# Kernel tuning notes

Hardware: AMD Instinct MI355X
Metric: run time of the kernel (lower is better)

Reference implementation:

```python
import jax, jax.numpy as jnp
import numpy as np

VIS_DIM, HID_DIM, ATT_DIM = 1024, 512, 256
B, R = 512, 196


def setup_inputs() -> dict:
    key = jax.random.key(0)
    ks = jax.random.split(key, 8)
    s_v = 1.0 / np.sqrt(VIS_DIM)
    s_h = 1.0 / np.sqrt(HID_DIM)
    s_a = 1.0 / np.sqrt(ATT_DIM)
    return {
        "visual_features": jax.random.normal(ks[0], (B, R, VIS_DIM), jnp.float32),
        "hidden_state": jax.random.normal(ks[1], (B, HID_DIM), jnp.float32),
        "Wv": jax.random.uniform(ks[2], (VIS_DIM, ATT_DIM), jnp.float32, -s_v, s_v),
        "bv": jax.random.uniform(ks[3], (ATT_DIM,), jnp.float32, -s_v, s_v),
        "Wh": jax.random.uniform(ks[4], (HID_DIM, ATT_DIM), jnp.float32, -s_h, s_h),
        "bh": jax.random.uniform(ks[5], (ATT_DIM,), jnp.float32, -s_h, s_h),
        "Wa": jax.random.uniform(ks[6], (ATT_DIM,), jnp.float32, -s_a, s_a),
        "ba": jax.random.uniform(ks[7], (), jnp.float32, -s_a, s_a),
    }


def reference(visual_features, hidden_state, Wv, bv, Wh, bh, Wa, ba):
    # visual_features: [B, R, Dv]; hidden_state: [B, Dh]
    v_proj = jnp.einsum('brd,da->bra', visual_features, Wv) + bv   # [B, R, A]
    h_proj = hidden_state @ Wh + bh                                # [B, A]
    joint = jax.nn.relu(v_proj + h_proj[:, None, :])               # [B, R, A]
    scores = jnp.einsum('bra,a->br', joint, Wa) + ba               # [B, R]
    att = jax.nn.softmax(scores, axis=1)                           # softmax over regions
    att_output = jnp.einsum('br,brd->bd', att, visual_features)    # [B, Dv]
    return att_output
```

## Files before the change

kernel.cpp:

```cpp
#include <hip/hip_runtime.h>
#include <stdint.h>
#include <stddef.h>

#define BATCH 512
#define RSZ   196
#define DV    1024
#define DH    512
#define DA    256
#define MTOT  (BATCH * RSZ)

typedef short short8 __attribute__((ext_vector_type(8)));
typedef float f32x4 __attribute__((ext_vector_type(4)));

static __device__ __forceinline__ short f2bf(float f) {
    union { float f; unsigned u; } x; x.f = f;
    unsigned r = x.u + 0x7fffu + ((x.u >> 16) & 1u);
    return (short)(r >> 16);
}

__global__ void k_prep_wvt(const float* __restrict__ Wv, short* __restrict__ WvT) {
    int idx = blockIdx.x * 256 + threadIdx.x;
    int k = idx >> 8;
    int n = idx & 255;
    WvT[n * DV + k] = f2bf(Wv[idx]);
}

__global__ __launch_bounds__(256) void k_hproj(const float* __restrict__ hs,
                                               const float* __restrict__ Wh,
                                               const float* __restrict__ bh,
                                               const float* __restrict__ bv,
                                               float* __restrict__ H) {
    __shared__ float sh[DH];
    int b = blockIdx.x, a = threadIdx.x;
    sh[a]       = hs[b * DH + a];
    sh[a + 256] = hs[b * DH + 256 + a];
    __syncthreads();
    float acc = 0.f;
#pragma unroll 8
    for (int k = 0; k < DH; ++k) acc += sh[k] * Wh[k * DA + a];
    H[b * DA + a] = acc + bh[a] + bv[a];
}

#define BK  64
#define LDA 72

__global__ __launch_bounds__(256) void k_scores(const float* __restrict__ vf,
                                                const short* __restrict__ WvT,
                                                const float* __restrict__ H,
                                                const float* __restrict__ Wa,
                                                const float* __restrict__ ba,
                                                float* __restrict__ scores) {
    __shared__ short As[64 * LDA];
    __shared__ short Bs[256 * LDA];
    __shared__ float sWa[DA];
    __shared__ float sH[2][DA];
    __shared__ float red[64][4];

    const int tid  = threadIdx.x;
    const int lane = tid & 63;
    const int w    = tid >> 6;
    const int ln   = lane & 15;
    const int q    = lane >> 4;
    const int m0   = blockIdx.x * 64;
    const int b0   = m0 / RSZ;
    const int b1   = (m0 + 63) / RSZ;

    sWa[tid]   = Wa[tid];
    sH[0][tid] = H[b0 * DA + tid];
    sH[1][tid] = H[b1 * DA + tid];

    f32x4 acc[4][4];
#pragma unroll
    for (int i = 0; i < 4; ++i)
#pragma unroll
        for (int j = 0; j < 4; ++j) acc[i][j] = (f32x4){0.f, 0.f, 0.f, 0.f};

    const int ar = tid >> 2;
    const int ac = (tid & 3) * 16;
    const float* aptr = vf + (size_t)(m0 + ar) * DV + ac;

    for (int kt = 0; kt < DV; kt += BK) {
        float4 av0 = *(const float4*)(aptr + kt + 0);
        float4 av1 = *(const float4*)(aptr + kt + 4);
        float4 av2 = *(const float4*)(aptr + kt + 8);
        float4 av3 = *(const float4*)(aptr + kt + 12);
        short8 p0 = { f2bf(av0.x), f2bf(av0.y), f2bf(av0.z), f2bf(av0.w),
                      f2bf(av1.x), f2bf(av1.y), f2bf(av1.z), f2bf(av1.w) };
        short8 p1 = { f2bf(av2.x), f2bf(av2.y), f2bf(av2.z), f2bf(av2.w),
                      f2bf(av3.x), f2bf(av3.y), f2bf(av3.z), f2bf(av3.w) };
        *(short8*)&As[ar * LDA + ac + 0] = p0;
        *(short8*)&As[ar * LDA + ac + 8] = p1;
#pragma unroll
        for (int j = 0; j < 8; ++j) {
            int c  = tid + 256 * j;
            int n  = c >> 3;
            int ko = (c & 7) * 8;
            *(short8*)&Bs[n * LDA + ko] = *(const short8*)(WvT + n * DV + kt + ko);
        }
        __syncthreads();
#pragma unroll
        for (int kk = 0; kk < 2; ++kk) {
            short8 afr[4], bfr[4];
#pragma unroll
            for (int i = 0; i < 4; ++i)
                afr[i] = *(short8*)&As[(i * 16 + ln) * LDA + kk * 32 + q * 8];
#pragma unroll
            for (int j = 0; j < 4; ++j)
                bfr[j] = *(short8*)&Bs[(w * 64 + j * 16 + ln) * LDA + kk * 32 + q * 8];
#pragma unroll
            for (int i = 0; i < 4; ++i)
#pragma unroll
                for (int j = 0; j < 4; ++j)
                    acc[i][j] = __builtin_amdgcn_mfma_f32_16x16x32_bf16(
                        afr[i], bfr[j], acc[i][j], 0, 0, 0);
        }
        __syncthreads();
    }

#pragma unroll
    for (int i = 0; i < 4; ++i) {
#pragma unroll
        for (int r = 0; r < 4; ++r) {
            int row = i * 16 + q * 4 + r;
            int m   = m0 + row;
            int bb  = m / RSZ;
            const float* hrow = sH[(bb == b0) ? 0 : 1];
            float p = 0.f;
#pragma unroll
            for (int j = 0; j < 4; ++j) {
                int a   = w * 64 + j * 16 + ln;
                float v = acc[i][j][r] + hrow[a];
                p += fmaxf(v, 0.f) * sWa[a];
            }
            p += __shfl_xor(p, 1);
            p += __shfl_xor(p, 2);
            p += __shfl_xor(p, 4);
            p += __shfl_xor(p, 8);
            if (ln == 0) red[row][w] = p;
        }
    }
    __syncthreads();
    if (tid < 64) {
        float s = red[tid][0] + red[tid][1] + red[tid][2] + red[tid][3] + ba[0];
        scores[m0 + tid] = s;
    }
}

__global__ __launch_bounds__(64) void k_softmax(const float* __restrict__ scores,
                                                float* __restrict__ att) {
    int b = blockIdx.x, t = threadIdx.x;
    float v[4], e[4];
    float m = -1e30f;
#pragma unroll
    for (int j = 0; j < 4; ++j) {
        int idx = j * 64 + t;
        v[j] = (idx < RSZ) ? scores[b * RSZ + idx] : -1e30f;
        m = fmaxf(m, v[j]);
    }
#pragma unroll
    for (int mk = 32; mk >= 1; mk >>= 1) m = fmaxf(m, __shfl_xor(m, mk));
    float s = 0.f;
#pragma unroll
    for (int j = 0; j < 4; ++j) {
        int idx = j * 64 + t;
        e[j] = (idx < RSZ) ? expf(v[j] - m) : 0.f;
        s += e[j];
    }
#pragma unroll
    for (int mk = 32; mk >= 1; mk >>= 1) s += __shfl_xor(s, mk);
    float inv = 1.f / s;
#pragma unroll
    for (int j = 0; j < 4; ++j) {
        int idx = j * 64 + t;
        if (idx < RSZ) att[b * RSZ + idx] = e[j] * inv;
    }
}

__global__ __launch_bounds__(256) void k_attout(const float* __restrict__ vf,
                                                const float* __restrict__ att,
                                                float* __restrict__ out) {
    __shared__ float satt[RSZ];
    int b = blockIdx.x, t = threadIdx.x;
    if (t < RSZ) satt[t] = att[b * RSZ + t];
    __syncthreads();
    const float4* vp = (const float4*)(vf + (size_t)b * RSZ * DV) + t;
    float4 acc = {0.f, 0.f, 0.f, 0.f};
    for (int r = 0; r < RSZ; r += 4) {
        float4 v0 = vp[(r + 0) * (DV / 4)];
        float4 v1 = vp[(r + 1) * (DV / 4)];
        float4 v2 = vp[(r + 2) * (DV / 4)];
        float4 v3 = vp[(r + 3) * (DV / 4)];
        float a0 = satt[r], a1 = satt[r + 1], a2 = satt[r + 2], a3 = satt[r + 3];
        acc.x += a0 * v0.x + a1 * v1.x + a2 * v2.x + a3 * v3.x;
        acc.y += a0 * v0.y + a1 * v1.y + a2 * v2.y + a3 * v3.y;
        acc.z += a0 * v0.z + a1 * v1.z + a2 * v2.z + a3 * v3.z;
        acc.w += a0 * v0.w + a1 * v1.w + a2 * v2.w + a3 * v3.w;
    }
    ((float4*)(out + (size_t)b * DV))[t] = acc;
}

extern "C" void kernel_launch(void* const* d_in, const int* in_sizes, int n_in,
                              void* d_out, int out_size, void* d_ws, size_t ws_size,
                              hipStream_t stream) {
    const float* vf = (const float*)d_in[0];
    const float* hs = (const float*)d_in[1];
    const float* Wv = (const float*)d_in[2];
    const float* bv = (const float*)d_in[3];
    const float* Wh = (const float*)d_in[4];
    const float* bh = (const float*)d_in[5];
    const float* Wa = (const float*)d_in[6];
    const float* ba = (const float*)d_in[7];
    float* out = (float*)d_out;

    char* ws = (char*)d_ws;
    short* WvT    = (short*)(ws);
    float* H      = (float*)(ws + (512 << 10));
    float* scores = (float*)(ws + (1024 << 10));
    float* att    = (float*)(ws + (1536 << 10));

    k_prep_wvt<<<1024, 256, 0, stream>>>(Wv, WvT);
    k_hproj<<<BATCH, 256, 0, stream>>>(hs, Wh, bh, bv, H);
    k_scores<<<MTOT / 64, 256, 0, stream>>>(vf, WvT, H, Wa, ba, scores);
    k_softmax<<<BATCH, 64, 0, stream>>>(scores, att);
    k_attout<<<BATCH, 256, 0, stream>>>(vf, att, out);
}
```

Measured before the change: 688.7 us.

## Enlarge score GEMM tile, async LDS loads for weights, fuse prep and softmax kernels

```diff
diff --git a/kernel.cpp b/kernel.cpp
--- a/kernel.cpp
+++ b/kernel.cpp
@@ -1,4 +1,5 @@
 #include <hip/hip_runtime.h>
+#include <hip/hip_bf16.h>
 #include <stdint.h>
 #include <stddef.h>
 
@@ -18,113 +19,146 @@
     return (short)(r >> 16);
 }
 
-__global__ void k_prep_wvt(const float* __restrict__ Wv, short* __restrict__ WvT) {
-    int idx = blockIdx.x * 256 + threadIdx.x;
-    int k = idx >> 8;
-    int n = idx & 255;
-    WvT[n * DV + k] = f2bf(Wv[idx]);
-}
-
-__global__ __launch_bounds__(256) void k_hproj(const float* __restrict__ hs,
-                                               const float* __restrict__ Wh,
-                                               const float* __restrict__ bh,
-                                               const float* __restrict__ bv,
-                                               float* __restrict__ H) {
-    __shared__ float sh[DH];
-    int b = blockIdx.x, a = threadIdx.x;
-    sh[a]       = hs[b * DH + a];
-    sh[a + 256] = hs[b * DH + 256 + a];
-    __syncthreads();
-    float acc = 0.f;
+static __device__ __forceinline__ int pk2(float x, float y) {
+    float2 f; f.x = x; f.y = y;
+    __hip_bfloat162 h = __float22bfloat162_rn(f);
+    int r; __builtin_memcpy(&r, &h, 4); return r;
+}
+
+static __device__ __forceinline__ void gl_lds16(const short* g, short* s) {
+    __builtin_amdgcn_global_load_lds(
+        (const __attribute__((address_space(1))) void*)g,
+        (__attribute__((address_space(3))) void*)s, 16, 0, 0);
+}
+
+__global__ __launch_bounds__(256) void k_prep(const float* __restrict__ Wv,
+                                              const float* __restrict__ hs,
+                                              const float* __restrict__ Wh,
+                                              const float* __restrict__ bh,
+                                              const float* __restrict__ bv,
+                                              short* __restrict__ WvT,
+                                              float* __restrict__ H) {
+    int tid = threadIdx.x;
+    if (blockIdx.x < 64) {
+        __shared__ short tile[16][DA];
+        int k0 = blockIdx.x * 16;
+#pragma unroll
+        for (int r = 0; r < 16; ++r)
+            tile[r][tid] = f2bf(Wv[(size_t)(k0 + r) * DA + tid]);
+        __syncthreads();
+        short o[16];
+#pragma unroll
+        for (int r = 0; r < 16; ++r) o[r] = tile[r][tid];
+        *(short8*)&WvT[(size_t)tid * DV + k0]     = *(short8*)&o[0];
+        *(short8*)&WvT[(size_t)tid * DV + k0 + 8] = *(short8*)&o[8];
+    } else {
+        __shared__ float sh[DH];
+        int b = blockIdx.x - 64, a = tid;
+        sh[a]       = hs[b * DH + a];
+        sh[a + 256] = hs[b * DH + 256 + a];
+        __syncthreads();
+        float acc = 0.f;
 #pragma unroll 8
-    for (int k = 0; k < DH; ++k) acc += sh[k] * Wh[k * DA + a];
-    H[b * DA + a] = acc + bh[a] + bv[a];
-}
-
+        for (int k = 0; k < DH; ++k) acc += sh[k] * Wh[k * DA + a];
+        H[b * DA + a] = acc + bh[a] + bv[a];
+    }
+}
+
+#define BM  128
+#define BN  256
 #define BK  64
 #define LDA 72
 
-__global__ __launch_bounds__(256) void k_scores(const float* __restrict__ vf,
-                                                const short* __restrict__ WvT,
-                                                const float* __restrict__ H,
-                                                const float* __restrict__ Wa,
-                                                const float* __restrict__ ba,
-                                                float* __restrict__ scores) {
-    __shared__ short As[64 * LDA];
-    __shared__ short Bs[256 * LDA];
+__global__ __launch_bounds__(256, 2) void k_scores(const float* __restrict__ vf,
+                                                   const short* __restrict__ WvT,
+                                                   const float* __restrict__ H,
+                                                   const float* __restrict__ Wa,
+                                                   const float* __restrict__ ba,
+                                                   float* __restrict__ scores) {
+    __shared__ short As[BM * LDA];
+    __shared__ short Bs[BN * BK];
     __shared__ float sWa[DA];
     __shared__ float sH[2][DA];
-    __shared__ float red[64][4];
-
-    const int tid  = threadIdx.x;
-    const int lane = tid & 63;
-    const int w    = tid >> 6;
-    const int ln   = lane & 15;
-    const int q    = lane >> 4;
-    const int m0   = blockIdx.x * 64;
-    const int b0   = m0 / RSZ;
-    const int b1   = (m0 + 63) / RSZ;
+    __shared__ float red[BM][4];
+
+    const int tid = threadIdx.x;
+    const int l   = tid & 63;
+    const int w   = tid >> 6;
+    const int ln  = l & 15;
+    const int q   = l >> 4;
+    const int m0  = blockIdx.x * BM;
+    const int b0  = m0 / RSZ;
+    const int bL  = (m0 + BM - 1) / RSZ;
 
     sWa[tid]   = Wa[tid];
     sH[0][tid] = H[b0 * DA + tid];
-    sH[1][tid] = H[b1 * DA + tid];
-
-    f32x4 acc[4][4];
-#pragma unroll
-    for (int i = 0; i < 4; ++i)
+    sH[1][tid] = H[bL * DA + tid];
+
+    f32x4 acc[8][4];
+#pragma unroll
+    for (int i = 0; i < 8; ++i)
 #pragma unroll
         for (int j = 0; j < 4; ++j) acc[i][j] = (f32x4){0.f, 0.f, 0.f, 0.f};
 
-    const int ar = tid >> 2;
-    const int ac = (tid & 3) * 16;
-    const float* aptr = vf + (size_t)(m0 + ar) * DV + ac;
+    const int ar = tid >> 1;
+    const int ac = (tid & 1) * 32;
+    const float4* ap = (const float4*)(vf + (size_t)(m0 + ar) * DV + ac);
+    short* awr = &As[ar * LDA + ac];
+
+    const int g   = l >> 3;
+    const int c   = l & 7;
+    const int csw = c ^ g;
+    const short* bsrc = WvT + (size_t)(w * 64 + g) * DV + csw * 8;
+    short* bdst = &Bs[(w * 8) * 512];
 
     for (int kt = 0; kt < DV; kt += BK) {
-        float4 av0 = *(const float4*)(aptr + kt + 0);
-        float4 av1 = *(const float4*)(aptr + kt + 4);
-        float4 av2 = *(const float4*)(aptr + kt + 8);
-        float4 av3 = *(const float4*)(aptr + kt + 12);
-        short8 p0 = { f2bf(av0.x), f2bf(av0.y), f2bf(av0.z), f2bf(av0.w),
-                      f2bf(av1.x), f2bf(av1.y), f2bf(av1.z), f2bf(av1.w) };
-        short8 p1 = { f2bf(av2.x), f2bf(av2.y), f2bf(av2.z), f2bf(av2.w),
-                      f2bf(av3.x), f2bf(av3.y), f2bf(av3.z), f2bf(av3.w) };
-        *(short8*)&As[ar * LDA + ac + 0] = p0;
-        *(short8*)&As[ar * LDA + ac + 8] = p1;
-#pragma unroll
-        for (int j = 0; j < 8; ++j) {
-            int c  = tid + 256 * j;
-            int n  = c >> 3;
-            int ko = (c & 7) * 8;
-            *(short8*)&Bs[n * LDA + ko] = *(const short8*)(WvT + n * DV + kt + ko);
-        }
+#pragma unroll
+        for (int j = 0; j < 8; ++j)
+            gl_lds16(bsrc + (size_t)j * 8 * DV + kt, bdst + j * 512);
+        int kb = kt >> 2;
+        float4 f0 = ap[kb + 0], f1 = ap[kb + 1], f2 = ap[kb + 2], f3 = ap[kb + 3];
+        float4 f4 = ap[kb + 4], f5 = ap[kb + 5], f6 = ap[kb + 6], f7 = ap[kb + 7];
+        union { short8 v; int i[4]; } u0, u1, u2, u3;
+        u0.i[0] = pk2(f0.x, f0.y); u0.i[1] = pk2(f0.z, f0.w);
+        u0.i[2] = pk2(f1.x, f1.y); u0.i[3] = pk2(f1.z, f1.w);
+        u1.i[0] = pk2(f2.x, f2.y); u1.i[1] = pk2(f2.z, f2.w);
+        u1.i[2] = pk2(f3.x, f3.y); u1.i[3] = pk2(f3.z, f3.w);
+        u2.i[0] = pk2(f4.x, f4.y); u2.i[1] = pk2(f4.z, f4.w);
+        u2.i[2] = pk2(f5.x, f5.y); u2.i[3] = pk2(f5.z, f5.w);
+        u3.i[0] = pk2(f6.x, f6.y); u3.i[1] = pk2(f6.z, f6.w);
+        u3.i[2] = pk2(f7.x, f7.y); u3.i[3] = pk2(f7.z, f7.w);
+        *(short8*)&awr[0]  = u0.v;
+        *(short8*)&awr[8]  = u1.v;
+        *(short8*)&awr[16] = u2.v;
+        *(short8*)&awr[24] = u3.v;
         __syncthreads();
 #pragma unroll
         for (int kk = 0; kk < 2; ++kk) {
-            short8 afr[4], bfr[4];
-#pragma unroll
-            for (int i = 0; i < 4; ++i)
-                afr[i] = *(short8*)&As[(i * 16 + ln) * LDA + kk * 32 + q * 8];
-#pragma unroll
-            for (int j = 0; j < 4; ++j)
-                bfr[j] = *(short8*)&Bs[(w * 64 + j * 16 + ln) * LDA + kk * 32 + q * 8];
-#pragma unroll
-            for (int i = 0; i < 4; ++i)
+            short8 bfr[4];
+#pragma unroll
+            for (int j = 0; j < 4; ++j) {
+                int n = w * 64 + j * 16 + ln;
+                bfr[j] = *(short8*)&Bs[n * BK + ((4 * kk + q) ^ (ln & 7)) * 8];
+            }
+#pragma unroll
+            for (int i = 0; i < 8; ++i) {
+                short8 afr = *(short8*)&As[(i * 16 + ln) * LDA + kk * 32 + q * 8];
 #pragma unroll
                 for (int j = 0; j < 4; ++j)
                     acc[i][j] = __builtin_amdgcn_mfma_f32_16x16x32_bf16(
-                        afr[i], bfr[j], acc[i][j], 0, 0, 0);
+                        afr, bfr[j], acc[i][j], 0, 0, 0);
+            }
         }
         __syncthreads();
     }
 
 #pragma unroll
-    for (int i = 0; i < 4; ++i) {
+    for (int i = 0; i < 8; ++i) {
 #pragma unroll
         for (int r = 0; r < 4; ++r) {
             int row = i * 16 + q * 4 + r;
-            int m   = m0 + row;
-            int bb  = m / RSZ;
-            const float* hrow = sH[(bb == b0) ? 0 : 1];
+            int bb  = (unsigned)(m0 + row) / RSZ;
+            const float* hrow = sH[bb - b0];
             float p = 0.f;
 #pragma unroll
             for (int j = 0; j < 4; ++j) {
@@ -140,49 +174,37 @@
         }
     }
     __syncthreads();
-    if (tid < 64) {
-        float s = red[tid][0] + red[tid][1] + red[tid][2] + red[tid][3] + ba[0];
-        scores[m0 + tid] = s;
-    }
-}
-
-__global__ __launch_bounds__(64) void k_softmax(const float* __restrict__ scores,
-                                                float* __restrict__ att) {
-    int b = blockIdx.x, t = threadIdx.x;
-    float v[4], e[4];
-    float m = -1e30f;
-#pragma unroll
-    for (int j = 0; j < 4; ++j) {
-        int idx = j * 64 + t;
-        v[j] = (idx < RSZ) ? scores[b * RSZ + idx] : -1e30f;
-        m = fmaxf(m, v[j]);
-    }
+    if (tid < BM) {
+        scores[m0 + tid] = red[tid][0] + red[tid][1] + red[tid][2] + red[tid][3] + ba[0];
+    }
+}
+
+__global__ __launch_bounds__(256) void k_out(const float* __restrict__ vf,
+                                             const float* __restrict__ scores,
+                                             float* __restrict__ out) {
+    __shared__ float satt[RSZ];
+    __shared__ float wrm[4];
+    __shared__ float wrs[4];
+    const int b = blockIdx.x, t = threadIdx.x;
+    const int l = t & 63, w = t >> 6;
+
+    float v = (t < RSZ) ? scores[b * RSZ + t] : -1e30f;
+    float m = v;
 #pragma unroll
     for (int mk = 32; mk >= 1; mk >>= 1) m = fmaxf(m, __shfl_xor(m, mk));
-    float s = 0.f;
-#pragma unroll
-    for (int j = 0; j < 4; ++j) {
-        int idx = j * 64 + t;
-        e[j] = (idx < RSZ) ? expf(v[j] - m) : 0.f;
-        s += e[j];
-    }
+    if (l == 0) wrm[w] = m;
+    __syncthreads();
+    m = fmaxf(fmaxf(wrm[0], wrm[1]), fmaxf(wrm[2], wrm[3]));
+    float e = (t < RSZ) ? expf(v - m) : 0.f;
+    float s = e;
 #pragma unroll
     for (int mk = 32; mk >= 1; mk >>= 1) s += __shfl_xor(s, mk);
-    float inv = 1.f / s;
-#pragma unroll
-    for (int j = 0; j < 4; ++j) {
-        int idx = j * 64 + t;
-        if (idx < RSZ) att[b * RSZ + idx] = e[j] * inv;
-    }
-}
-
-__global__ __launch_bounds__(256) void k_attout(const float* __restrict__ vf,
-                                                const float* __restrict__ att,
-                                                float* __restrict__ out) {
-    __shared__ float satt[RSZ];
-    int b = blockIdx.x, t = threadIdx.x;
-    if (t < RSZ) satt[t] = att[b * RSZ + t];
-    __syncthreads();
+    if (l == 0) wrs[w] = s;
+    __syncthreads();
+    s = wrs[0] + wrs[1] + wrs[2] + wrs[3];
+    if (t < RSZ) satt[t] = e / s;
+    __syncthreads();
+
     const float4* vp = (const float4*)(vf + (size_t)b * RSZ * DV) + t;
     float4 acc = {0.f, 0.f, 0.f, 0.f};
     for (int r = 0; r < RSZ; r += 4) {
@@ -216,11 +238,8 @@
     short* WvT    = (short*)(ws);
     float* H      = (float*)(ws + (512 << 10));
     float* scores = (float*)(ws + (1024 << 10));
-    float* att    = (float*)(ws + (1536 << 10));
-
-    k_prep_wvt<<<1024, 256, 0, stream>>>(Wv, WvT);
-    k_hproj<<<BATCH, 256, 0, stream>>>(hs, Wh, bh, bv, H);
-    k_scores<<<MTOT / 64, 256, 0, stream>>>(vf, WvT, H, Wa, ba, scores);
-    k_softmax<<<BATCH, 64, 0, stream>>>(scores, att);
-    k_attout<<<BATCH, 256, 0, stream>>>(vf, att, out);
-}
+
+    k_prep<<<576, 256, 0, stream>>>(Wv, hs, Wh, bh, bv, WvT, H);
+    k_scores<<<MTOT / BM, 256, 0, stream>>>(vf, WvT, H, Wa, ba, scores);
+    k_out<<<BATCH, 256, 0, stream>>>(vf, scores, out);
+}
```

Measured after the change: 695.7 us. About the same (+1.0%).
